# Kernel optimization log

Hardware: AMD Instinct MI355X
Metric: run time of the kernel (lower is better)

The kernel has to match this reference:

```python
import jax, jax.numpy as jnp
import numpy as np

D_MODEL = 1024
N_HEAD = 16
T = 2048
HEAD = D_MODEL // N_HEAD  # 64
RANKS = [32, 16, 8, 8]
BLOCKS = [2048, 1024, 512, 256]  # seq_len // 2**i ('default')
OFFS = np.cumsum([0] + RANKS)


def setup_inputs() -> dict:
    key = jax.random.key(0)
    k0, k1, k2 = jax.random.split(key, 3)
    s = 0.02
    x = jax.random.normal(k0, (1, T, D_MODEL), dtype=jnp.float32)
    W_attn = jax.random.normal(k1, (D_MODEL, 3 * D_MODEL), dtype=jnp.float32) * s
    b_attn = jnp.zeros((3 * D_MODEL,), dtype=jnp.float32)
    W_proj = jax.random.normal(k2, (D_MODEL, D_MODEL), dtype=jnp.float32) * s
    b_proj = jnp.zeros((D_MODEL,), dtype=jnp.float32)
    return {"x": x, "W_attn": W_attn, "b_attn": b_attn, "W_proj": W_proj, "b_proj": b_proj}


def reference(x, W_attn, b_attn, W_proj, b_proj):
    B = x.shape[0]
    qkv = x @ W_attn + b_attn  # (B,T,3*D)
    q, k, v = jnp.split(qkv, 3, axis=-1)
    # (B,H,T,HEAD)
    q = q.reshape(B, T, N_HEAD, HEAD).transpose(0, 2, 1, 3)
    k = k.reshape(B, T, N_HEAD, HEAD).transpose(0, 2, 1, 3)
    v = v.reshape(B, T, N_HEAD, HEAD).transpose(0, 2, 1, 3)

    att = jnp.zeros((B, N_HEAD, T, T), dtype=x.dtype)
    for i, (bdx, r) in enumerate(zip(BLOCKS, RANKS)):
        nb = T // bdx
        qi = q[..., OFFS[i]:OFFS[i + 1]].reshape(B, N_HEAD, nb, bdx, r)
        ki = k[..., OFFS[i]:OFFS[i + 1]].reshape(B, N_HEAD, nb, bdx, r)
        blk = jnp.einsum('bhnir,bhnjr->bhnij', qi, ki) * (1.0 / r)  # (B,H,nb,bdx,bdx)
        # scatter block-diagonal scores into full T x T matrix
        att5 = att.reshape(B, N_HEAD, nb, bdx, nb, bdx)
        ar = jnp.arange(nb)
        att5 = att5.at[:, :, ar, :, ar, :].add(jnp.moveaxis(blk, 2, 0))
        att = att5.reshape(B, N_HEAD, T, T)

    causal = jnp.tril(jnp.ones((T, T), dtype=bool))
    att = jnp.where(causal, att, -jnp.inf)
    att = jax.nn.softmax(att, axis=-1)
    y = att @ v  # (B,H,T,HEAD)
    y = y.transpose(0, 2, 1, 3).reshape(B, T, D_MODEL)
    return y @ W_proj + b_proj
```

## Files before the change

kernel.cpp:

```cpp
#include <hip/hip_runtime.h>

using bf16x8 = __attribute__((ext_vector_type(8))) short;
using f32x4  = __attribute__((ext_vector_type(4))) float;

#define DEVI __device__ __forceinline__

DEVI unsigned short f2bf(float f) {
  union { float ff; unsigned u; } v; v.ff = f;
  unsigned r = v.u + 0x7FFFu + ((v.u >> 16) & 1u);
  return (unsigned short)(r >> 16);
}

DEVI int cvtpk(float lo, float hi) {
  int r;
  asm("v_cvt_pk_bf16_f32 %0, %1, %2" : "=v"(r) : "v"(lo), "v"(hi));
  return r;
}

DEVI void g2l16(const void* g, void* l) {
  __builtin_amdgcn_global_load_lds(
      (const __attribute__((address_space(1))) unsigned int*)g,
      (__attribute__((address_space(3))) unsigned int*)l, 16, 0, 0);
}

__global__ void k_convx(const float* __restrict__ in, unsigned short* __restrict__ out, int n4) {
  int i = blockIdx.x * 256 + threadIdx.x;
  if (i >= n4) return;
  float4 v = reinterpret_cast<const float4*>(in)[i];
  ushort4 o;
  o.x = f2bf(v.x); o.y = f2bf(v.y); o.z = f2bf(v.z); o.w = f2bf(v.w);
  reinterpret_cast<ushort4*>(out)[i] = o;
}

__global__ void k_tconv(const float* __restrict__ in, unsigned short* __restrict__ out, int R, int C) {
  __shared__ float tile[32][33];
  int c0 = blockIdx.x * 32, r0 = blockIdx.y * 32;
  int x = threadIdx.x, y = threadIdx.y;
  for (int i = y; i < 32; i += 8) tile[i][x] = in[(size_t)(r0 + i) * C + c0 + x];
  __syncthreads();
  for (int i = y; i < 32; i += 8) out[(size_t)(c0 + i) * R + r0 + x] = f2bf(tile[x][i]);
}

__global__ __launch_bounds__(256) void k_gemm_qkv(
    const unsigned short* __restrict__ A, const unsigned short* __restrict__ Bt,
    const float* __restrict__ bias,
    unsigned short* __restrict__ qs, unsigned short* __restrict__ kbuf,
    unsigned short* __restrict__ vT) {
  constexpr int K = 1024;
  __shared__ __align__(16) unsigned short As[128 * 64];
  __shared__ __align__(16) unsigned short Bs[128 * 64];
  const int lane = threadIdx.x & 63, wid = threadIdx.x >> 6;
  const int m0 = blockIdx.y * 128, n0 = blockIdx.x * 128;
  const int wr = (wid >> 1) * 64, wc = (wid & 1) * 64;
  const int g = lane >> 4, li = lane & 15;
  f32x4 acc[4][4] = {};
  for (int k0 = 0; k0 < K; k0 += 64) {
    __syncthreads();
    for (int c = wid; c < 16; c += 4) {
      const int fb = c * 1024;
      const int flat = fb + lane * 16;
      const int row = flat >> 7, colb = flat & 127;
      g2l16((const char*)A  + ((size_t)(m0 + row) * K + k0) * 2 + colb, (char*)As + fb);
      g2l16((const char*)Bt + ((size_t)(n0 + row) * K + k0) * 2 + colb, (char*)Bs + fb);
    }
    __syncthreads();
#pragma unroll
    for (int ks = 0; ks < 2; ks++) {
      const int kk = ks * 32 + g * 8;
      bf16x8 a[4], b[4];
#pragma unroll
      for (int i = 0; i < 4; i++)
        a[i] = *reinterpret_cast<const bf16x8*>(As + (wr + i * 16 + li) * 64 + kk);
#pragma unroll
      for (int j = 0; j < 4; j++)
        b[j] = *reinterpret_cast<const bf16x8*>(Bs + (wc + j * 16 + li) * 64 + kk);
#pragma unroll
      for (int i = 0; i < 4; i++)
#pragma unroll
        for (int j = 0; j < 4; j++)
          acc[i][j] = __builtin_amdgcn_mfma_f32_16x16x32_bf16(a[i], b[j], acc[i][j], 0, 0, 0);
    }
  }
  const int rb = m0 + wr + g * 4;
  const int cb = n0 + wc + li;
#pragma unroll
  for (int j = 0; j < 4; j++) {
    const int c = cb + j * 16;
    const float bv = bias[c];
    const int hq = c >> 6, d = c & 63;
    const float sc = d < 32 ? 0.03125f : (d < 48 ? 0.0625f : 0.125f);
#pragma unroll
    for (int i = 0; i < 4; i++) {
#pragma unroll
      for (int r = 0; r < 4; r++) {
        const int t = rb + i * 16 + r;
        const float val = acc[i][j][r] + bv;
        if (c < 1024) {
          qs[((size_t)(hq * 2048 + t) << 6) + d] = f2bf(val * sc);
        } else if (c < 2048) {
          kbuf[((size_t)((hq - 16) * 2048 + t) << 6) + d] = f2bf(val);
        } else {
          vT[(size_t)((hq - 32) * 64 + d) * 2048 + t] = f2bf(val);
        }
      }
    }
  }
}

DEVI int chunk_off(int qt) {
  const int off[17] = {0,1,2,3,4,6,8,10,12,15,18,21,24,28,32,36,40};
  return off[qt];
}

__global__ __launch_bounds__(256) void k_attn_part(
    const unsigned short* __restrict__ qs, const unsigned short* __restrict__ kbuf,
    const unsigned short* __restrict__ vT,
    float* __restrict__ o_part, float* __restrict__ ml) {
  __shared__ __align__(16) unsigned short Ks[128 * 64];
  __shared__ __align__(16) unsigned short Vs[64 * 128];
  const int lane = threadIdx.x & 63, wid = threadIdx.x >> 6;
  const int g = lane >> 4, li = lane & 15;

  const int h = blockIdx.x / 40;
  const int rem = blockIdx.x % 40;
  int qt = 0;
#pragma unroll
  for (int i = 0; i < 16; i++)
    if (rem >= chunk_off(i + 1)) qt = i + 1;
  const int ci = rem - chunk_off(qt);
  const int kt0 = ci * 4;
  const int kt1 = min(qt, kt0 + 3);
  const int q0 = qt * 128;

  const bf16x8 bzero = {0, 0, 0, 0, 0, 0, 0, 0};

  bf16x8 qf[2][2];
#pragma unroll
  for (int mi = 0; mi < 2; mi++)
#pragma unroll
    for (int ks = 0; ks < 2; ks++) {
      const int t = q0 + wid * 32 + mi * 16 + li;
      const int d = ks * 32 + g * 8;
      qf[mi][ks] = *reinterpret_cast<const bf16x8*>(qs + ((size_t)(h * 2048 + t) << 6) + d);
    }

  f32x4 o[2][4] = {};
  float m_run[2] = {-1e30f, -1e30f}, l_run[2] = {0.f, 0.f};

  const int q256 = qt >> 1;
  for (int kt = kt0; kt <= kt1; kt++) {
    __syncthreads();
    for (int c = wid; c < 16; c += 4) {
      const int fb = c * 1024;
      const int flat = fb + lane * 16;
      {
        const int row = flat >> 7;
        const int cs = (((flat >> 4) & 7) ^ (row & 7)) << 4;
        g2l16((const char*)kbuf + (((size_t)(h * 2048 + kt * 128 + row)) << 7) + cs,
              (char*)Ks + fb);
      }
      {
        const int row = flat >> 8;
        const int cs = (((flat >> 4) & 15) ^ (row & 15)) << 4;
        g2l16((const char*)vT + ((size_t)(h * 64 + row) * 2048 + kt * 128) * 2 + cs,
              (char*)Vs + fb);
      }
    }
    __syncthreads();

    const int x = q256 ^ (kt >> 1);
    const int Keff = (x == 0) ? 64 : ((x >= 4) ? 32 : ((x >= 2) ? 48 : 56));

    f32x4 st[8][2] = {};
#pragma unroll
    for (int cf = 0; cf < 8; cf++) {
      const int krow = cf * 16 + li;
      const bf16x8 a0 = *reinterpret_cast<const bf16x8*>(
          Ks + krow * 64 + ((g ^ (krow & 7)) << 3));
      st[cf][0] = __builtin_amdgcn_mfma_f32_16x16x32_bf16(a0, qf[0][0], st[cf][0], 0, 0, 0);
      st[cf][1] = __builtin_amdgcn_mfma_f32_16x16x32_bf16(a0, qf[1][0], st[cf][1], 0, 0, 0);
    }
    if (Keff > 32) {
      const bool zf = (32 + g * 8) >= Keff;
#pragma unroll
      for (int cf = 0; cf < 8; cf++) {
        const int krow = cf * 16 + li;
        bf16x8 a1 = *reinterpret_cast<const bf16x8*>(
            Ks + krow * 64 + (((4 + g) ^ (krow & 7)) << 3));
        if (zf) a1 = bzero;
        st[cf][0] = __builtin_amdgcn_mfma_f32_16x16x32_bf16(a1, qf[0][1], st[cf][0], 0, 0, 0);
        st[cf][1] = __builtin_amdgcn_mfma_f32_16x16x32_bf16(a1, qf[1][1], st[cf][1], 0, 0, 0);
      }
    }

    if (kt == qt) {
#pragma unroll
      for (int cf = 0; cf < 8; cf++)
#pragma unroll
        for (int mi = 0; mi < 2; mi++)
#pragma unroll
          for (int r = 0; r < 4; r++) {
            const int t2 = cf * 16 + g * 4 + r;
            const int qq = wid * 32 + mi * 16 + li;
            if (t2 > qq) st[cf][mi][r] = -1e30f;
          }
    }

    int pk[2][8][2];
    float corrb[2][4];
#pragma unroll
    for (int mi = 0; mi < 2; mi++) {
      float tm = st[0][mi][0];
#pragma unroll
      for (int cf = 0; cf < 8; cf++)
#pragma unroll
        for (int r = 0; r < 4; r++)
          if (cf | r) tm = fmaxf(tm, st[cf][mi][r]);
      tm = fmaxf(tm, __shfl_xor(tm, 16));
      tm = fmaxf(tm, __shfl_xor(tm, 32));
      const float mn = fmaxf(m_run[mi], tm);
      const float corr = __expf(m_run[mi] - mn);
      m_run[mi] = mn;
      float sum = 0.f;
#pragma unroll
      for (int cf = 0; cf < 8; cf++) {
        const float p0 = __expf(st[cf][mi][0] - mn);
        const float p1 = __expf(st[cf][mi][1] - mn);
        const float p2 = __expf(st[cf][mi][2] - mn);
        const float p3 = __expf(st[cf][mi][3] - mn);
        sum += (p0 + p1) + (p2 + p3);
        pk[mi][cf][0] = cvtpk(p0, p1);
        pk[mi][cf][1] = cvtpk(p2, p3);
      }
      sum += __shfl_xor(sum, 16);
      sum += __shfl_xor(sum, 32);
      l_run[mi] = l_run[mi] * corr + sum;
      corrb[mi][0] = __shfl(corr, 4 * g + 0);
      corrb[mi][1] = __shfl(corr, 4 * g + 1);
      corrb[mi][2] = __shfl(corr, 4 * g + 2);
      corrb[mi][3] = __shfl(corr, 4 * g + 3);
    }
#pragma unroll
    for (int mi = 0; mi < 2; mi++)
#pragma unroll
      for (int nf = 0; nf < 4; nf++)
#pragma unroll
        for (int r = 0; r < 4; r++)
          o[mi][nf][r] *= corrb[mi][r];

#pragma unroll
    for (int ks2 = 0; ks2 < 4; ks2++) {
      bf16x8 pa[2];
#pragma unroll
      for (int mi = 0; mi < 2; mi++) {
        union { int i[4]; bf16x8 v; } u;
        u.i[0] = pk[mi][2 * ks2][0];
        u.i[1] = pk[mi][2 * ks2][1];
        u.i[2] = pk[mi][2 * ks2 + 1][0];
        u.i[3] = pk[mi][2 * ks2 + 1][1];
        pa[mi] = u.v;
      }
      bf16x8 vb[4];
#pragma unroll
      for (int nf = 0; nf < 4; nf++) {
        const int vrow = nf * 16 + li;
        const int rm = vrow & 15;
        const int ch0 = 4 * ks2 + (g >> 1);
        const int b8 = (g & 1) * 8;
        union { struct { int2 lo, hi; } p; bf16x8 v; } u;
        u.p.lo = *reinterpret_cast<const int2*>(
            (const char*)Vs + vrow * 256 + (((ch0 + 0) ^ rm) << 4) + b8);
        u.p.hi = *reinterpret_cast<const int2*>(
            (const char*)Vs + vrow * 256 + (((ch0 + 2) ^ rm) << 4) + b8);
        vb[nf] = u.v;
      }
#pragma unroll
      for (int mi = 0; mi < 2; mi++)
#pragma unroll
        for (int nf = 0; nf < 4; nf++)
          o[mi][nf] = __builtin_amdgcn_mfma_f32_16x16x32_bf16(pa[mi], vb[nf], o[mi][nf], 0, 0, 0);
    }
  }

  const size_t pbase = (size_t)blockIdx.x * 8192;
#pragma unroll
  for (int mi = 0; mi < 2; mi++) {
#pragma unroll
    for (int nf = 0; nf < 4; nf++)
#pragma unroll
      for (int r = 0; r < 4; r++) {
        const int row = wid * 32 + mi * 16 + g * 4 + r;
        o_part[pbase + (size_t)row * 64 + nf * 16 + li] = o[mi][nf][r];
      }
  }
  if (g == 0) {
#pragma unroll
    for (int mi = 0; mi < 2; mi++) {
      const int row = wid * 32 + mi * 16 + li;
      ml[(size_t)blockIdx.x * 256 + row] = m_run[mi];
      ml[(size_t)blockIdx.x * 256 + 128 + row] = l_run[mi];
    }
  }
}

__global__ __launch_bounds__(256) void k_combine(
    const float* __restrict__ o_part, const float* __restrict__ ml,
    unsigned short* __restrict__ yb) {
  const int h = blockIdx.x >> 4, qt = blockIdx.x & 15;
  const int nc = (qt >> 2) + 1;
  const int base = h * 40 + chunk_off(qt);
  const int row = threadIdx.x >> 1;
  const int c0 = (threadIdx.x & 1) * 32;

  float m_i[4], l_i[4];
  float M = -1e30f;
  for (int ci = 0; ci < nc; ci++) {
    m_i[ci] = ml[(size_t)(base + ci) * 256 + row];
    l_i[ci] = ml[(size_t)(base + ci) * 256 + 128 + row];
    M = fmaxf(M, m_i[ci]);
  }
  float L = 0.f, w[4];
  for (int ci = 0; ci < nc; ci++) {
    w[ci] = __expf(m_i[ci] - M);
    L += w[ci] * l_i[ci];
  }
  const float inv = 1.0f / L;

  float acc[32];
#pragma unroll
  for (int j = 0; j < 32; j++) acc[j] = 0.f;
  for (int ci = 0; ci < nc; ci++) {
    const float* src = o_part + (size_t)(base + ci) * 8192 + (size_t)row * 64 + c0;
    const float wc = w[ci];
#pragma unroll
    for (int j4 = 0; j4 < 8; j4++) {
      float4 v = reinterpret_cast<const float4*>(src)[j4];
      acc[j4 * 4 + 0] += wc * v.x;
      acc[j4 * 4 + 1] += wc * v.y;
      acc[j4 * 4 + 2] += wc * v.z;
      acc[j4 * 4 + 3] += wc * v.w;
    }
  }
  const int t = qt * 128 + row;
  unsigned short* dst = yb + (size_t)t * 1024 + h * 64 + c0;
#pragma unroll
  for (int j8 = 0; j8 < 4; j8++) {
    ushort4 pk;
    pk.x = f2bf(acc[j8 * 8 + 0] * inv);
    pk.y = f2bf(acc[j8 * 8 + 1] * inv);
    pk.z = f2bf(acc[j8 * 8 + 2] * inv);
    pk.w = f2bf(acc[j8 * 8 + 3] * inv);
    ushort4 pk2;
    pk2.x = f2bf(acc[j8 * 8 + 4] * inv);
    pk2.y = f2bf(acc[j8 * 8 + 5] * inv);
    pk2.z = f2bf(acc[j8 * 8 + 6] * inv);
    pk2.w = f2bf(acc[j8 * 8 + 7] * inv);
    reinterpret_cast<ushort4*>(dst)[j8 * 2 + 0] = pk;
    reinterpret_cast<ushort4*>(dst)[j8 * 2 + 1] = pk2;
  }
}

__global__ __launch_bounds__(256) void k_gemm_proj(
    const unsigned short* __restrict__ A, const unsigned short* __restrict__ Bt,
    const float* __restrict__ bias, float* __restrict__ out) {
  constexpr int K = 1024;
  __shared__ __align__(16) unsigned short As[128 * 64];
  __shared__ __align__(16) unsigned short Bs[128 * 64];
  const int lane = threadIdx.x & 63, wid = threadIdx.x >> 6;
  const int m0 = blockIdx.y * 128, n0 = blockIdx.x * 128;
  const int wr = (wid >> 1) * 64, wc = (wid & 1) * 64;
  const int g = lane >> 4, li = lane & 15;
  f32x4 acc[4][4] = {};
  for (int k0 = 0; k0 < K; k0 += 64) {
    __syncthreads();
    for (int c = wid; c < 16; c += 4) {
      const int fb = c * 1024;
      const int flat = fb + lane * 16;
      const int row = flat >> 7, colb = flat & 127;
      g2l16((const char*)A  + ((size_t)(m0 + row) * K + k0) * 2 + colb, (char*)As + fb);
      g2l16((const char*)Bt + ((size_t)(n0 + row) * K + k0) * 2 + colb, (char*)Bs + fb);
    }
    __syncthreads();
#pragma unroll
    for (int ks = 0; ks < 2; ks++) {
      const int kk = ks * 32 + g * 8;
      bf16x8 a[4], b[4];
#pragma unroll
      for (int i = 0; i < 4; i++)
        a[i] = *reinterpret_cast<const bf16x8*>(As + (wr + i * 16 + li) * 64 + kk);
#pragma unroll
      for (int j = 0; j < 4; j++)
        b[j] = *reinterpret_cast<const bf16x8*>(Bs + (wc + j * 16 + li) * 64 + kk);
#pragma unroll
      for (int i = 0; i < 4; i++)
#pragma unroll
        for (int j = 0; j < 4; j++)
          acc[i][j] = __builtin_amdgcn_mfma_f32_16x16x32_bf16(a[i], b[j], acc[i][j], 0, 0, 0);
    }
  }
  const int rb = m0 + wr + g * 4;
  const int cb = n0 + wc + li;
#pragma unroll
  for (int j = 0; j < 4; j++) {
    const int c = cb + j * 16;
    const float bv = bias[c];
#pragma unroll
    for (int i = 0; i < 4; i++) {
#pragma unroll
      for (int r = 0; r < 4; r++) {
        const int t = rb + i * 16 + r;
        out[(size_t)t * 1024 + c] = acc[i][j][r] + bv;
      }
    }
  }
}

extern "C" void kernel_launch(void* const* d_in, const int* in_sizes, int n_in,
                              void* d_out, int out_size, void* d_ws, size_t ws_size,
                              hipStream_t stream) {
  const float* x      = (const float*)d_in[0];
  const float* W_attn = (const float*)d_in[1];
  const float* b_attn = (const float*)d_in[2];
  const float* W_proj = (const float*)d_in[3];
  const float* b_proj = (const float*)d_in[4];
  float* out = (float*)d_out;
  char* ws = (char*)d_ws;
  const size_t MB = 1024 * 1024;
  unsigned short* xb  = (unsigned short*)(ws + 0 * MB);
  unsigned short* WaT = (unsigned short*)(ws + 4 * MB);
  unsigned short* WpT = (unsigned short*)(ws + 10 * MB);
  unsigned short* qs  = (unsigned short*)(ws + 12 * MB);
  unsigned short* kb  = (unsigned short*)(ws + 16 * MB);
  unsigned short* vT  = (unsigned short*)(ws + 20 * MB);
  unsigned short* yb  = (unsigned short*)(ws + 24 * MB);
  float* o_part = (float*)(ws + 28 * MB);
  float* ml     = (float*)(ws + 48 * MB + 256 * 1024);

  k_convx<<<dim3(2048), dim3(256), 0, stream>>>(x, xb, 524288);
  k_tconv<<<dim3(96, 32), dim3(32, 8), 0, stream>>>(W_attn, WaT, 1024, 3072);
  k_tconv<<<dim3(32, 32), dim3(32, 8), 0, stream>>>(W_proj, WpT, 1024, 1024);
  k_gemm_qkv<<<dim3(24, 16), dim3(256), 0, stream>>>(xb, WaT, b_attn, qs, kb, vT);
  k_attn_part<<<dim3(640), dim3(256), 0, stream>>>(qs, kb, vT, o_part, ml);
  k_combine<<<dim3(256), dim3(256), 0, stream>>>(o_part, ml, yb);
  k_gemm_proj<<<dim3(8, 16), dim3(256), 0, stream>>>(yb, WpT, b_proj, out);
}
```

Before: 110.3 us.

## Double-buffer LDS staging and shrink tiles in QKV and projection GEMMs

Both GEMM kernels now prefetch the next K-slice into a second LDS buffer while computing on the current one, which removes one barrier per iteration and overlaps global-to-LDS loads with MFMA work. Tile sizes also shrink: QKV goes to 128x64 tiles (768 blocks) and the projection to 64x64 tiles (512 blocks). The smaller tiles are meant to fill all CUs on the MI355X, at the cost of less data reuse per block and more total global traffic.

```diff
diff --git a/kernel.cpp b/kernel.cpp
--- a/kernel.cpp
+++ b/kernel.cpp
@@ -47,44 +47,61 @@
     unsigned short* __restrict__ qs, unsigned short* __restrict__ kbuf,
     unsigned short* __restrict__ vT) {
   constexpr int K = 1024;
-  __shared__ __align__(16) unsigned short As[128 * 64];
-  __shared__ __align__(16) unsigned short Bs[128 * 64];
+  __shared__ __align__(16) unsigned short As[2][128 * 64];
+  __shared__ __align__(16) unsigned short Bs[2][64 * 64];
   const int lane = threadIdx.x & 63, wid = threadIdx.x >> 6;
-  const int m0 = blockIdx.y * 128, n0 = blockIdx.x * 128;
-  const int wr = (wid >> 1) * 64, wc = (wid & 1) * 64;
+  const int m0 = blockIdx.y * 128, n0 = blockIdx.x * 64;
+  const int wr = (wid >> 1) * 64, wc = (wid & 1) * 32;
   const int g = lane >> 4, li = lane & 15;
-  f32x4 acc[4][4] = {};
-  for (int k0 = 0; k0 < K; k0 += 64) {
-    __syncthreads();
-    for (int c = wid; c < 16; c += 4) {
-      const int fb = c * 1024;
-      const int flat = fb + lane * 16;
-      const int row = flat >> 7, colb = flat & 127;
-      g2l16((const char*)A  + ((size_t)(m0 + row) * K + k0) * 2 + colb, (char*)As + fb);
-      g2l16((const char*)Bt + ((size_t)(n0 + row) * K + k0) * 2 + colb, (char*)Bs + fb);
-    }
-    __syncthreads();
+  f32x4 acc[4][2] = {};
+
+#define STAGE_QKV(buf, k0)                                                              \
+  {                                                                                     \
+    _Pragma("unroll")                                                                   \
+    for (int c = wid * 4; c < wid * 4 + 4; c++) {                                       \
+      const int flat = c * 1024 + lane * 16;                                            \
+      const int row = flat >> 7, colb = flat & 127;                                     \
+      g2l16((const char*)A + ((size_t)(m0 + row) * K + (k0)) * 2 + colb,                \
+            (char*)As[buf] + c * 1024);                                                 \
+    }                                                                                   \
+    _Pragma("unroll")                                                                   \
+    for (int c = wid * 2; c < wid * 2 + 2; c++) {                                       \
+      const int flat = c * 1024 + lane * 16;                                            \
+      const int row = flat >> 7, colb = flat & 127;                                     \
+      g2l16((const char*)Bt + ((size_t)(n0 + row) * K + (k0)) * 2 + colb,               \
+            (char*)Bs[buf] + c * 1024);                                                 \
+    }                                                                                   \
+  }
+
+  STAGE_QKV(0, 0);
+  __syncthreads();
+  int buf = 0;
+  for (int t = 0; t < 16; t++) {
+    if (t < 15) STAGE_QKV(buf ^ 1, (t + 1) * 64);
 #pragma unroll
     for (int ks = 0; ks < 2; ks++) {
       const int kk = ks * 32 + g * 8;
-      bf16x8 a[4], b[4];
+      bf16x8 a[4], b[2];
 #pragma unroll
       for (int i = 0; i < 4; i++)
-        a[i] = *reinterpret_cast<const bf16x8*>(As + (wr + i * 16 + li) * 64 + kk);
-#pragma unroll
-      for (int j = 0; j < 4; j++)
-        b[j] = *reinterpret_cast<const bf16x8*>(Bs + (wc + j * 16 + li) * 64 + kk);
+        a[i] = *reinterpret_cast<const bf16x8*>(As[buf] + (wr + i * 16 + li) * 64 + kk);
+#pragma unroll
+      for (int j = 0; j < 2; j++)
+        b[j] = *reinterpret_cast<const bf16x8*>(Bs[buf] + (wc + j * 16 + li) * 64 + kk);
 #pragma unroll
       for (int i = 0; i < 4; i++)
 #pragma unroll
-        for (int j = 0; j < 4; j++)
+        for (int j = 0; j < 2; j++)
           acc[i][j] = __builtin_amdgcn_mfma_f32_16x16x32_bf16(a[i], b[j], acc[i][j], 0, 0, 0);
     }
-  }
+    __syncthreads();
+    buf ^= 1;
+  }
+
   const int rb = m0 + wr + g * 4;
   const int cb = n0 + wc + li;
 #pragma unroll
-  for (int j = 0; j < 4; j++) {
+  for (int j = 0; j < 2; j++) {
     const int c = cb + j * 16;
     const float bv = bias[c];
     const int hq = c >> 6, d = c & 63;
@@ -105,6 +122,7 @@
       }
     }
   }
+#undef STAGE_QKV
 }
 
 DEVI int chunk_off(int qt) {
@@ -364,48 +382,60 @@
     const unsigned short* __restrict__ A, const unsigned short* __restrict__ Bt,
     const float* __restrict__ bias, float* __restrict__ out) {
   constexpr int K = 1024;
-  __shared__ __align__(16) unsigned short As[128 * 64];
-  __shared__ __align__(16) unsigned short Bs[128 * 64];
+  __shared__ __align__(16) unsigned short As[2][64 * 64];
+  __shared__ __align__(16) unsigned short Bs[2][64 * 64];
   const int lane = threadIdx.x & 63, wid = threadIdx.x >> 6;
-  const int m0 = blockIdx.y * 128, n0 = blockIdx.x * 128;
-  const int wr = (wid >> 1) * 64, wc = (wid & 1) * 64;
+  const int m0 = blockIdx.y * 64, n0 = blockIdx.x * 64;
+  const int wr = (wid >> 1) * 32, wc = (wid & 1) * 32;
   const int g = lane >> 4, li = lane & 15;
-  f32x4 acc[4][4] = {};
-  for (int k0 = 0; k0 < K; k0 += 64) {
-    __syncthreads();
-    for (int c = wid; c < 16; c += 4) {
-      const int fb = c * 1024;
-      const int flat = fb + lane * 16;
-      const int row = flat >> 7, colb = flat & 127;
-      g2l16((const char*)A  + ((size_t)(m0 + row) * K + k0) * 2 + colb, (char*)As + fb);
-      g2l16((const char*)Bt + ((size_t)(n0 + row) * K + k0) * 2 + colb, (char*)Bs + fb);
-    }
-    __syncthreads();
+  f32x4 acc[2][2] = {};
+
+#define STAGE_PROJ(buf, k0)                                                             \
+  {                                                                                     \
+    _Pragma("unroll")                                                                   \
+    for (int c = wid * 2; c < wid * 2 + 2; c++) {                                       \
+      const int flat = c * 1024 + lane * 16;                                            \
+      const int row = flat >> 7, colb = flat & 127;                                     \
+      g2l16((const char*)A + ((size_t)(m0 + row) * K + (k0)) * 2 + colb,                \
+            (char*)As[buf] + c * 1024);                                                 \
+      g2l16((const char*)Bt + ((size_t)(n0 + row) * K + (k0)) * 2 + colb,               \
+            (char*)Bs[buf] + c * 1024);                                                 \
+    }                                                                                   \
+  }
+
+  STAGE_PROJ(0, 0);
+  __syncthreads();
+  int buf = 0;
+  for (int t = 0; t < 16; t++) {
+    if (t < 15) STAGE_PROJ(buf ^ 1, (t + 1) * 64);
 #pragma unroll
     for (int ks = 0; ks < 2; ks++) {
       const int kk = ks * 32 + g * 8;
-      bf16x8 a[4], b[4];
-#pragma unroll
-      for (int i = 0; i < 4; i++)
-        a[i] = *reinterpret_cast<const bf16x8*>(As + (wr + i * 16 + li) * 64 + kk);
-#pragma unroll
-      for (int j = 0; j < 4; j++)
-        b[j] = *reinterpret_cast<const bf16x8*>(Bs + (wc + j * 16 + li) * 64 + kk);
-#pragma unroll
-      for (int i = 0; i < 4; i++)
-#pragma unroll
-        for (int j = 0; j < 4; j++)
+      bf16x8 a[2], b[2];
+#pragma unroll
+      for (int i = 0; i < 2; i++)
+        a[i] = *reinterpret_cast<const bf16x8*>(As[buf] + (wr + i * 16 + li) * 64 + kk);
+#pragma unroll
+      for (int j = 0; j < 2; j++)
+        b[j] = *reinterpret_cast<const bf16x8*>(Bs[buf] + (wc + j * 16 + li) * 64 + kk);
+#pragma unroll
+      for (int i = 0; i < 2; i++)
+#pragma unroll
+        for (int j = 0; j < 2; j++)
           acc[i][j] = __builtin_amdgcn_mfma_f32_16x16x32_bf16(a[i], b[j], acc[i][j], 0, 0, 0);
     }
-  }
+    __syncthreads();
+    buf ^= 1;
+  }
+
   const int rb = m0 + wr + g * 4;
   const int cb = n0 + wc + li;
 #pragma unroll
-  for (int j = 0; j < 4; j++) {
+  for (int j = 0; j < 2; j++) {
     const int c = cb + j * 16;
     const float bv = bias[c];
 #pragma unroll
-    for (int i = 0; i < 4; i++) {
+    for (int i = 0; i < 2; i++) {
 #pragma unroll
       for (int r = 0; r < 4; r++) {
         const int t = rb + i * 16 + r;
@@ -413,6 +443,7 @@
       }
     }
   }
+#undef STAGE_PROJ
 }
 
 extern "C" void kernel_launch(void* const* d_in, const int* in_sizes, int n_in,
@@ -439,8 +470,8 @@
   k_convx<<<dim3(2048), dim3(256), 0, stream>>>(x, xb, 524288);
   k_tconv<<<dim3(96, 32), dim3(32, 8), 0, stream>>>(W_attn, WaT, 1024, 3072);
   k_tconv<<<dim3(32, 32), dim3(32, 8), 0, stream>>>(W_proj, WpT, 1024, 1024);
-  k_gemm_qkv<<<dim3(24, 16), dim3(256), 0, stream>>>(xb, WaT, b_attn, qs, kb, vT);
+  k_gemm_qkv<<<dim3(48, 16), dim3(256), 0, stream>>>(xb, WaT, b_attn, qs, kb, vT);
   k_attn_part<<<dim3(640), dim3(256), 0, stream>>>(qs, kb, vT, o_part, ml);
   k_combine<<<dim3(256), dim3(256), 0, stream>>>(o_part, ml, yb);
-  k_gemm_proj<<<dim3(8, 16), dim3(256), 0, stream>>>(yb, WpT, b_proj, out);
-}
+  k_gemm_proj<<<dim3(16, 32), dim3(256), 0, stream>>>(yb, WpT, b_proj, out);
+}
```

New measurement: 103.7 us. -5.9%, faster.
